# Kernel optimization log

Hardware: AMD Instinct MI355X
Metric: run time of the kernel (lower is better)

The kernel has to match this reference:

```python
import jax, jax.numpy as jnp
import numpy as np

NUM_HEADS = 16
NEG_INF = -1e30


def setup_inputs() -> dict:
    key = jax.random.key(0)
    k1, k2, k3 = jax.random.split(key, 3)
    B, S, D = 2, 2048, 1024
    x = jax.random.normal(k1, (B, S, D), dtype=jnp.float32)
    # torch Linear(D, 3D, bias=False) stored here already transposed: y = x @ w_qkv
    w_qkv = jax.random.normal(k2, (D, 3 * D), dtype=jnp.float32) * 0.02
    w_out = jax.random.normal(k3, (D, D), dtype=jnp.float32) * 0.02
    return {"x": x, "w_qkv": w_qkv, "w_out": w_out}


def reference(x, w_qkv, w_out):
    B, S, D = x.shape
    H = NUM_HEADS
    dh = D // H
    qkv = x @ w_qkv                      # [B, S, 3D]
    q, k, v = jnp.split(qkv, 3, axis=-1)

    def to_heads(t):
        return t.reshape(B, S, H, dh).transpose(0, 2, 1, 3)  # [B, H, S, dh]

    q, k, v = to_heads(q), to_heads(k), to_heads(v)
    scale = jnp.asarray(dh, x.dtype) ** -0.5
    scores = jnp.einsum('bhqd,bhkd->bhqk', q, k) * scale     # [B, H, S, S]
    causal = jnp.tril(jnp.ones((S, S), dtype=bool))
    scores = jnp.where(causal, scores, NEG_INF)
    attn = jax.nn.softmax(scores, axis=-1)
    out = jnp.einsum('bhqk,bhkd->bhqd', attn, v)             # [B, H, S, dh]
    out = out.transpose(0, 2, 1, 3).reshape(B, S, D)
    return out @ w_out
```

## Files before the change

### kernel.cpp

```cpp
#include <hip/hip_runtime.h>

typedef unsigned short u16;
typedef unsigned int u32;

typedef __bf16 bf16x8 __attribute__((ext_vector_type(8)));
typedef _Float16 f16x8 __attribute__((ext_vector_type(8)));
typedef float f32x4 __attribute__((ext_vector_type(4)));

typedef __attribute__((address_space(1))) u32 as1_u32;
typedef __attribute__((address_space(3))) u32 as3_u32;

#define EKF 0.18033688011112042f

__device__ __forceinline__ u16 f2bf(float x) {
  u32 u = __float_as_uint(x);
  u = u + 0x7fffu + ((u >> 16) & 1u);
  return (u16)(u >> 16);
}
__device__ __forceinline__ u32 pack2(float a, float b) {
  return (u32)f2bf(a) | ((u32)f2bf(b) << 16);
}
__device__ __forceinline__ u32 pkf16(float a, float b) {
  return __builtin_bit_cast(u32, __builtin_amdgcn_cvt_pkrtz(a, b));
}
__device__ __forceinline__ u16 f2h(float a) {
  return (u16)(pkf16(a, a) & 0xffffu);
}
__device__ __forceinline__ void gld_lds16(const u16* g, const u16* l) {
  __builtin_amdgcn_global_load_lds((const as1_u32*)g, (as3_u32*)l, 16, 0, 0);
}

__global__ __launch_bounds__(256) void prepass_kernel(const float* __restrict__ x,
                                                      const float* __restrict__ w_qkv,
                                                      const float* __restrict__ w_out,
                                                      u16* __restrict__ xb,
                                                      u16* __restrict__ wqkvT,
                                                      u16* __restrict__ woutT) {
  __shared__ float tile[64][65];
  int bid = blockIdx.x;
  int t = threadIdx.x;
  if (bid < 4096) {
    int i = bid * 256 + t;
    float4 v = ((const float4*)x)[i];
    uint2 r;
    r.x = pack2(v.x, v.y);
    r.y = pack2(v.z, v.w);
    ((uint2*)xb)[i] = r;
    return;
  }
  const float* W;
  u16* WT;
  int K, N, bx, by;
  if (bid < 4096 + 768) {
    int b2 = bid - 4096;
    W = w_qkv; WT = wqkvT; K = 1024; N = 3072; bx = b2 & 15; by = b2 >> 4;
  } else {
    int b2 = bid - 4864;
    W = w_out; WT = woutT; K = 1024; N = 1024; bx = b2 & 15; by = b2 >> 4;
  }
  int k0 = bx * 64, n0 = by * 64;
  int r = t >> 4, c4 = (t & 15) * 4;
#pragma unroll
  for (int i = 0; i < 4; ++i) {
    int row = r + i * 16;
    float4 v = *(const float4*)&W[(size_t)(k0 + row) * N + n0 + c4];
    tile[row][c4 + 0] = v.x; tile[row][c4 + 1] = v.y;
    tile[row][c4 + 2] = v.z; tile[row][c4 + 3] = v.w;
  }
  __syncthreads();
#pragma unroll
  for (int i = 0; i < 4; ++i) {
    int n = r + i * 16;
    uint2 o;
    o.x = pack2(tile[c4 + 0][n], tile[c4 + 1][n]);
    o.y = pack2(tile[c4 + 2][n], tile[c4 + 3][n]);
    *(uint2*)&WT[(size_t)(n0 + n) * K + k0 + c4] = o;
  }
}

template <int OUT_MODE, int BN>
__global__ __launch_bounds__(256) void gemm_bt_kernel(const u16* __restrict__ A,
                                                      const u16* __restrict__ BT,
                                                      void* __restrict__ Cv,
                                                      u16* __restrict__ VT,
                                                      int M, int N, int K) {
  const int NF = (BN == 128) ? 4 : 2;
  __shared__ __attribute__((aligned(16))) u16 sA[128 * 32];
  __shared__ __attribute__((aligned(16))) u16 sB[BN * 32];
  const int tid = threadIdx.x;
  const int wave = tid >> 6;
  const int lane = tid & 63;
  const int bm = blockIdx.y * 128;
  const int bn = blockIdx.x * BN;
  const int wm = (wave >> 1) * 64;
  const int wn = (wave & 1) * (BN / 2);
  const int lr = lane & 15;
  const int kg = lane >> 4;

  const int srow = tid >> 2;
  const int scol = (tid & 3) * 8;
  const u16* pa0 = A + (size_t)(bm + srow) * K + scol;
  const u16* pa1 = pa0 + (size_t)64 * K;
  const u16* pb0 = BT + (size_t)(bn + srow) * K + scol;
  const u16* pb1 = pb0 + (size_t)64 * K;
  const u16* la = sA + wave * 512;
  const u16* lb = sB + wave * 512;

  f32x4 acc[4][NF];
#pragma unroll
  for (int i = 0; i < 4; i++)
#pragma unroll
    for (int j = 0; j < NF; j++) {
      f32x4 z = {0.f, 0.f, 0.f, 0.f};
      acc[i][j] = z;
    }

  for (int k0 = 0; k0 < K; k0 += 32) {
    __syncthreads();
    gld_lds16(pa0 + k0, la);
    gld_lds16(pa1 + k0, la + 2048);
    gld_lds16(pb0 + k0, lb);
    if (BN == 128) gld_lds16(pb1 + k0, lb + 2048);
    __syncthreads();
    bf16x8 af[4], bfr[NF];
#pragma unroll
    for (int mi = 0; mi < 4; mi++)
      af[mi] = *(const bf16x8*)(sA + (wm + mi * 16 + lr) * 32 + kg * 8);
#pragma unroll
    for (int ni = 0; ni < NF; ni++)
      bfr[ni] = *(const bf16x8*)(sB + (wn + ni * 16 + lr) * 32 + kg * 8);
#pragma unroll
    for (int mi = 0; mi < 4; mi++)
#pragma unroll
      for (int ni = 0; ni < NF; ni++)
        acc[mi][ni] = __builtin_amdgcn_mfma_f32_16x16x32_bf16(bfr[ni], af[mi], acc[mi][ni], 0, 0, 0);
  }

#pragma unroll
  for (int mi = 0; mi < 4; mi++)
#pragma unroll
    for (int ni = 0; ni < NF; ni++) {
      int r = bm + wm + mi * 16 + lr;
      int c0 = bn + wn + ni * 16 + kg * 4;
      f32x4 a = acc[mi][ni];
      if (OUT_MODE == 0) {
        float4 o = make_float4(a[0], a[1], a[2], a[3]);
        *(float4*)&((float*)Cv)[(size_t)r * N + c0] = o;
      } else {
        if (c0 < 1024) {
          uint2 o = make_uint2(pack2(a[0] * EKF, a[1] * EKF), pack2(a[2] * EKF, a[3] * EKF));
          *(uint2*)&((u16*)Cv)[(size_t)r * 2048 + c0] = o;
        } else if (c0 < 2048) {
          uint2 o = make_uint2(pack2(a[0], a[1]), pack2(a[2], a[3]));
          *(uint2*)&((u16*)Cv)[(size_t)r * 2048 + c0] = o;
        } else {
          int cc = c0 - 2048;
          int bh2 = (r >> 11) * 16 + (cc >> 6);
          int j = r & 2047;
          u16* vrow = VT + ((size_t)bh2 * 64 + (cc & 63)) * 2048 + j;
#pragma unroll
          for (int rr = 0; rr < 4; rr++)
            vrow[(size_t)rr * 2048] = f2h(a[rr]);
        }
      }
    }
}

__global__ __launch_bounds__(256, 4) void attn_mfma_kernel(const u16* __restrict__ qk,
                                                           const u16* __restrict__ vt,
                                                           u16* __restrict__ out) {
  __shared__ __attribute__((aligned(16))) u16 sK[2][64 * 64];
  __shared__ __attribute__((aligned(16))) u16 sV[2][64 * 64];
  __shared__ __attribute__((aligned(16))) u16 sP[4][16 * 64];

  const int tid = threadIdx.x;
  const int wave = tid >> 6;
  const int lane = tid & 63;
  const int lr = lane & 15;
  const int kg = lane >> 4;
  const int l7 = lr & 7;

  int idx = blockIdx.x;
  int qi = 31 - (idx >> 5);
  int bh = idx & 31;
  int b = bh >> 4, h = bh & 15;
  int q0 = qi * 64;

  const u16* qbase = qk + (size_t)b * 2048 * 2048 + h * 64;
  const u16* kbase = qbase + 1024;
  const u16* vbase = vt + (size_t)bh * 64 * 2048;
  u16* obase = out + (size_t)b * 2048 * 1024 + h * 64;

  const int sra = wave * 16 + (lane >> 3);
  const int srb = sra + 8;
  const int sc = lane & 7;
  const u32 koffA = (u32)sra * 2048 + (u32)((sc ^ (sra & 7)) * 8);
  const u32 koffB = (u32)srb * 2048 + (u32)((sc ^ (srb & 7)) * 8);
  const u32 ldsA = (wave * 2 + 0) * 512;
  const u32 ldsB = (wave * 2 + 1) * 512;

  const int qcol = q0 + wave * 16 + lr;
  bf16x8 qf0, qf1;
  {
    const u16* qrow = qbase + (size_t)qcol * 2048;
    qf0 = *(const bf16x8*)(qrow + kg * 8);
    qf1 = *(const bf16x8*)(qrow + 32 + kg * 8);
  }

  const u32 ka0 = (u32)(lr * 64 + ((kg ^ l7) * 8));
  const u32 ka1 = (u32)(lr * 64 + (((4 + kg) ^ l7) * 8));
  u16* const sPw = sP[wave];
  const u32 pr0 = (u32)(lr * 64 + (((kg * 2) ^ (l7 << 1)) * 4));
  const u32 pr1 = (u32)(lr * 64 + (((8 + kg * 2) ^ (l7 << 1)) * 4));

  f32x4 oacc[4];
#pragma unroll
  for (int i = 0; i < 4; ++i) {
    f32x4 z = {0.f, 0.f, 0.f, 0.f};
    oacc[i] = z;
  }
  float lsum = 0.f;

  const int nrounds = qi + 1;
  gld_lds16(kbase + koffA, sK[0] + ldsA);
  gld_lds16(kbase + koffB, sK[0] + ldsB);
  gld_lds16(vbase + koffA, sV[0] + ldsA);
  gld_lds16(vbase + koffB, sV[0] + ldsB);
  __syncthreads();

  for (int t = 0; t < nrounds; ++t) {
    if (t + 1 < nrounds) {
      int j1 = (t + 1) * 64;
      u16* dK = sK[(t + 1) & 1];
      u16* dV = sV[(t + 1) & 1];
      gld_lds16(kbase + (size_t)j1 * 2048 + koffA, dK + ldsA);
      gld_lds16(kbase + (size_t)j1 * 2048 + koffB, dK + ldsB);
      gld_lds16(vbase + j1 + koffA, dV + ldsA);
      gld_lds16(vbase + j1 + koffB, dV + ldsB);
    }
    const u16* sKb = sK[t & 1];
    const u16* sVb = sV[t & 1];
    const bool diag = (t == qi);

#pragma unroll
    for (int jt = 0; jt < 4; ++jt) {
      u16* pw = sPw + lr * 64 + (((jt * 4 + kg) ^ (l7 << 1)) * 4);
      if (!diag || jt <= wave) {
        bf16x8 kf0 = *(const bf16x8*)(sKb + jt * 1024 + ka0);
        bf16x8 kf1 = *(const bf16x8*)(sKb + jt * 1024 + ka1);
        f32x4 c = {0.f, 0.f, 0.f, 0.f};
        c = __builtin_amdgcn_mfma_f32_16x16x32_bf16(kf0, qf0, c, 0, 0, 0);
        c = __builtin_amdgcn_mfma_f32_16x16x32_bf16(kf1, qf1, c, 0, 0, 0);
        float p0 = exp2f(c[0]);
        float p1 = exp2f(c[1]);
        float p2 = exp2f(c[2]);
        float p3 = exp2f(c[3]);
        if (diag && jt == wave) {
          int jr = kg * 4;
          p0 = (jr + 0 <= lr) ? p0 : 0.f;
          p1 = (jr + 1 <= lr) ? p1 : 0.f;
          p2 = (jr + 2 <= lr) ? p2 : 0.f;
          p3 = (jr + 3 <= lr) ? p3 : 0.f;
        }
        lsum += (p0 + p1) + (p2 + p3);
        *(uint2*)pw = make_uint2(pkf16(p0, p1), pkf16(p2, p3));
      } else {
        *(uint2*)pw = make_uint2(0u, 0u);
      }
    }

    asm volatile("" ::: "memory");

    f16x8 pf0 = *(const f16x8*)(sPw + pr0);
    f16x8 pf1 = *(const f16x8*)(sPw + pr1);
#pragma unroll
    for (int dt = 0; dt < 4; ++dt) {
      f16x8 vf0 = *(const f16x8*)(sVb + dt * 1024 + ka0);
      f16x8 vf1 = *(const f16x8*)(sVb + dt * 1024 + ka1);
      oacc[dt] = __builtin_amdgcn_mfma_f32_16x16x32_f16(vf0, pf0, oacc[dt], 0, 0, 0);
      oacc[dt] = __builtin_amdgcn_mfma_f32_16x16x32_f16(vf1, pf1, oacc[dt], 0, 0, 0);
    }
    __syncthreads();
  }

  lsum += __shfl_xor(lsum, 16);
  lsum += __shfl_xor(lsum, 32);
  float inv = 1.0f / lsum;

  u16* orow = obase + (size_t)qcol * 1024;
#pragma unroll
  for (int dt = 0; dt < 4; ++dt) {
    uint2 o2 = make_uint2(pack2(oacc[dt][0] * inv, oacc[dt][1] * inv),
                          pack2(oacc[dt][2] * inv, oacc[dt][3] * inv));
    *(uint2*)(orow + dt * 16 + kg * 4) = o2;
  }
}

extern "C" void kernel_launch(void* const* d_in, const int* in_sizes, int n_in,
                              void* d_out, int out_size, void* d_ws, size_t ws_size,
                              hipStream_t stream) {
  const float* x = (const float*)d_in[0];
  const float* w_qkv = (const float*)d_in[1];
  const float* w_out = (const float*)d_in[2];
  float* out = (float*)d_out;

  char* ws = (char*)d_ws;
  u16* xb    = (u16*)(ws);
  u16* wqkvT = (u16*)(ws + (8u << 20));
  u16* woutT = (u16*)(ws + (14u << 20));
  u16* qkb   = (u16*)(ws + (16u << 20));
  u16* vtb   = (u16*)(ws + (32u << 20));
  u16* attn  = (u16*)(ws + (40u << 20));

  prepass_kernel<<<5120, 256, 0, stream>>>(x, w_qkv, w_out, xb, wqkvT, woutT);

  gemm_bt_kernel<2, 128><<<dim3(3072 / 128, 4096 / 128), 256, 0, stream>>>(
      xb, wqkvT, (void*)qkb, vtb, 4096, 3072, 1024);

  attn_mfma_kernel<<<1024, 256, 0, stream>>>(qkb, vtb, attn);

  gemm_bt_kernel<0, 64><<<dim3(1024 / 64, 4096 / 128), 256, 0, stream>>>(
      attn, woutT, (void*)out, nullptr, 4096, 1024, 1024);
}
```

Measured before the change: 184.1 us.

## Double GEMM K-step to 64 with XOR-swizzled LDS and staged coalesced epilogue

The GEMM main loop now loads 64-wide K slices per iteration, halving the barrier count, and stores them in LDS with an XOR swizzle to avoid bank conflicts on fragment reads. The fp32 output and bf16 Q/K outputs are staged through shared memory in two column halves, so each row is written with wide coalesced vector stores instead of scattered 16-byte pieces. This doubles the LDS footprint and adds extra barriers in the epilogue, which may reduce occupancy.

```diff
diff --git a/kernel.cpp b/kernel.cpp
--- a/kernel.cpp
+++ b/kernel.cpp
@@ -85,8 +85,8 @@
                                                       u16* __restrict__ VT,
                                                       int M, int N, int K) {
   const int NF = (BN == 128) ? 4 : 2;
-  __shared__ __attribute__((aligned(16))) u16 sA[128 * 32];
-  __shared__ __attribute__((aligned(16))) u16 sB[BN * 32];
+  __shared__ __attribute__((aligned(16))) u16 sA[128 * 64];
+  __shared__ __attribute__((aligned(16))) u16 sB[BN * 64];
   const int tid = threadIdx.x;
   const int wave = tid >> 6;
   const int lane = tid & 63;
@@ -96,13 +96,13 @@
   const int wn = (wave & 1) * (BN / 2);
   const int lr = lane & 15;
   const int kg = lane >> 4;
-
-  const int srow = tid >> 2;
-  const int scol = (tid & 3) * 8;
-  const u16* pa0 = A + (size_t)(bm + srow) * K + scol;
-  const u16* pa1 = pa0 + (size_t)64 * K;
-  const u16* pb0 = BT + (size_t)(bn + srow) * K + scol;
-  const u16* pb1 = pb0 + (size_t)64 * K;
+  const int lr7 = lr & 7;
+
+  const int sr = tid >> 3;
+  const int sc = tid & 7;
+  const int scg = (sc ^ (sr & 7)) * 8;
+  const u16* pa = A + (size_t)(bm + sr) * K + scg;
+  const u16* pb = BT + (size_t)(bn + sr) * K + scg;
   const u16* la = sA + wave * 512;
   const u16* lb = sB + wave * 512;
 
@@ -115,55 +115,103 @@
       acc[i][j] = z;
     }
 
-  for (int k0 = 0; k0 < K; k0 += 32) {
+  for (int k0 = 0; k0 < K; k0 += 64) {
     __syncthreads();
-    gld_lds16(pa0 + k0, la);
-    gld_lds16(pa1 + k0, la + 2048);
-    gld_lds16(pb0 + k0, lb);
-    if (BN == 128) gld_lds16(pb1 + k0, lb + 2048);
+#pragma unroll
+    for (int i = 0; i < 4; ++i)
+      gld_lds16(pa + (size_t)(i * 32) * K + k0, la + i * 2048);
+#pragma unroll
+    for (int i = 0; i < NF; ++i)
+      gld_lds16(pb + (size_t)(i * 32) * K + k0, lb + i * 2048);
     __syncthreads();
-    bf16x8 af[4], bfr[NF];
+#pragma unroll
+    for (int kk = 0; kk < 2; ++kk) {
+      bf16x8 af[4], bfr[NF];
+      const int ch = ((kk * 4 + kg) ^ lr7) * 8;
+#pragma unroll
+      for (int mi = 0; mi < 4; mi++)
+        af[mi] = *(const bf16x8*)(sA + (wm + mi * 16 + lr) * 64 + ch);
+#pragma unroll
+      for (int ni = 0; ni < NF; ni++)
+        bfr[ni] = *(const bf16x8*)(sB + (wn + ni * 16 + lr) * 64 + ch);
+#pragma unroll
+      for (int mi = 0; mi < 4; mi++)
+#pragma unroll
+        for (int ni = 0; ni < NF; ni++)
+          acc[mi][ni] = __builtin_amdgcn_mfma_f32_16x16x32_bf16(bfr[ni], af[mi], acc[mi][ni], 0, 0, 0);
+    }
+  }
+
+  if (OUT_MODE == 0) {
+    float* buf = (float*)sA;
+    float* outp = (float*)Cv;
+#pragma unroll
+    for (int hc = 0; hc < 2; ++hc) {
+      __syncthreads();
+      if ((wave & 1) == hc) {
+#pragma unroll
+        for (int mi = 0; mi < 4; mi++)
+#pragma unroll
+          for (int ni = 0; ni < NF; ni++) {
+            int row = wm + mi * 16 + lr;
+            int cp = ((ni * 4 + kg) ^ lr7) * 4;
+            *(f32x4*)(buf + row * 32 + cp) = acc[mi][ni];
+          }
+      }
+      __syncthreads();
+#pragma unroll
+      for (int i = 0; i < 4; ++i) {
+        int row = i * 32 + (tid >> 3);
+        int lc = tid & 7;
+        float4 v = *(const float4*)(buf + row * 32 + ((lc ^ (row & 7)) * 4));
+        *(float4*)(outp + (size_t)(bm + row) * N + bn + hc * 32 + lc * 4) = v;
+      }
+    }
+  } else if (bn >= 2048) {
 #pragma unroll
     for (int mi = 0; mi < 4; mi++)
-      af[mi] = *(const bf16x8*)(sA + (wm + mi * 16 + lr) * 32 + kg * 8);
-#pragma unroll
-    for (int ni = 0; ni < NF; ni++)
-      bfr[ni] = *(const bf16x8*)(sB + (wn + ni * 16 + lr) * 32 + kg * 8);
-#pragma unroll
-    for (int mi = 0; mi < 4; mi++)
-#pragma unroll
-      for (int ni = 0; ni < NF; ni++)
-        acc[mi][ni] = __builtin_amdgcn_mfma_f32_16x16x32_bf16(bfr[ni], af[mi], acc[mi][ni], 0, 0, 0);
-  }
-
-#pragma unroll
-  for (int mi = 0; mi < 4; mi++)
-#pragma unroll
-    for (int ni = 0; ni < NF; ni++) {
-      int r = bm + wm + mi * 16 + lr;
-      int c0 = bn + wn + ni * 16 + kg * 4;
-      f32x4 a = acc[mi][ni];
-      if (OUT_MODE == 0) {
-        float4 o = make_float4(a[0], a[1], a[2], a[3]);
-        *(float4*)&((float*)Cv)[(size_t)r * N + c0] = o;
-      } else {
-        if (c0 < 1024) {
-          uint2 o = make_uint2(pack2(a[0] * EKF, a[1] * EKF), pack2(a[2] * EKF, a[3] * EKF));
-          *(uint2*)&((u16*)Cv)[(size_t)r * 2048 + c0] = o;
-        } else if (c0 < 2048) {
-          uint2 o = make_uint2(pack2(a[0], a[1]), pack2(a[2], a[3]));
-          *(uint2*)&((u16*)Cv)[(size_t)r * 2048 + c0] = o;
-        } else {
-          int cc = c0 - 2048;
-          int bh2 = (r >> 11) * 16 + (cc >> 6);
-          int j = r & 2047;
-          u16* vrow = VT + ((size_t)bh2 * 64 + (cc & 63)) * 2048 + j;
-#pragma unroll
-          for (int rr = 0; rr < 4; rr++)
-            vrow[(size_t)rr * 2048] = f2h(a[rr]);
-        }
-      }
-    }
+#pragma unroll
+      for (int ni = 0; ni < NF; ni++) {
+        int r = bm + wm + mi * 16 + lr;
+        int cc = bn + wn + ni * 16 + kg * 4 - 2048;
+        int bh2 = (r >> 11) * 16 + (cc >> 6);
+        int j = r & 2047;
+        u16* vrow = VT + ((size_t)bh2 * 64 + (cc & 63)) * 2048 + j;
+        f32x4 a = acc[mi][ni];
+#pragma unroll
+        for (int rr = 0; rr < 4; rr++)
+          vrow[(size_t)rr * 2048] = f2h(a[rr]);
+      }
+  } else {
+    float scale = (bn < 1024) ? EKF : 1.0f;
+    u16* buf = sA;
+    u16* qkp = (u16*)Cv;
+#pragma unroll
+    for (int hc = 0; hc < 2; ++hc) {
+      __syncthreads();
+      if ((wave & 1) == hc) {
+#pragma unroll
+        for (int mi = 0; mi < 4; mi++)
+#pragma unroll
+          for (int ni = 0; ni < NF; ni++) {
+            int row = wm + mi * 16 + lr;
+            int sp = ((ni * 4 + kg) ^ (lr & 6)) * 4;
+            f32x4 a = acc[mi][ni];
+            *(uint2*)(buf + row * 64 + sp) =
+                make_uint2(pack2(a[0] * scale, a[1] * scale),
+                           pack2(a[2] * scale, a[3] * scale));
+          }
+      }
+      __syncthreads();
+#pragma unroll
+      for (int i = 0; i < 4; ++i) {
+        int row = i * 32 + (tid >> 3);
+        int lc = tid & 7;
+        uint4 v = *(const uint4*)(buf + row * 64 + (((2 * lc) ^ (row & 6)) * 4));
+        *(uint4*)(qkp + (size_t)(bm + row) * 2048 + bn + hc * 64 + lc * 8) = v;
+      }
+    }
+  }
 }
 
 __global__ __launch_bounds__(256, 4) void attn_mfma_kernel(const u16* __restrict__ qk,
```

Result: faster. 175.9 us (-4.4%).
